# Kernel optimization log

Hardware: AMD Instinct MI355X
Metric: run time of the kernel (lower is better)

## Reference

```python
import jax, jax.numpy as jnp
import numpy as np

N_NODES = 100000
N_EDGES = 1600000
FDIM = 128


def setup_inputs() -> dict:
    key = jax.random.key(0)
    k1, k2 = jax.random.split(key)
    x = jax.random.normal(k1, (N_NODES, FDIM), dtype=jnp.float32)
    edge_index = jax.random.randint(k2, (2, N_EDGES), 0, N_NODES, dtype=jnp.int64)
    # GCNConv params as loaded by the module: identity weight, zero bias
    W = jnp.eye(FDIM, dtype=jnp.float32)
    bias = jnp.zeros((FDIM,), dtype=jnp.float32)
    return {"x": x, "W": W, "bias": bias, "edge_index": edge_index}


def reference(x, W, bias, edge_index):
    n = x.shape[0]
    src, dst = edge_index[0], edge_index[1]
    # GCNConv default: add self-loops with weight 1.0
    loop = jnp.arange(n, dtype=edge_index.dtype)
    src_f = jnp.concatenate([src, loop])
    dst_f = jnp.concatenate([dst, loop])
    ew = jnp.ones(src_f.shape[0], dtype=x.dtype)
    # symmetric normalization: deg computed on destination (col)
    deg = jax.ops.segment_sum(ew, dst_f, num_segments=n)
    dinv = jnp.where(deg > 0, deg ** -0.5, 0.0).astype(x.dtype)
    norm = dinv[src_f] * dinv[dst_f]  # [E+n]
    h = x @ W.T  # linear transform (W = I here, but kept faithful)
    msg = h[src_f] * norm[:, None]  # gather + scale, [E+n, fdim]
    out = jax.ops.segment_sum(msg, dst_f, num_segments=n) + bias  # scatter-add
    return jnp.sum(out, axis=0, keepdims=True)  # [1, fdim]
```

## Files before the change

### kernel.cpp

```cpp
#include <hip/hip_runtime.h>

#define FD 128
#define CHD 32768
#define NSLD 64
#define CHS 16384
#define NSLS 32
#define RXB 512
#define QSCALE 16777216.0f
#define QINV   5.9604644775390625e-8f

__device__ __forceinline__ unsigned quant_w(int dp1) {
    return (unsigned)(rsqrtf((float)dp1) * QSCALE + 0.5f);
}

__device__ __forceinline__ bool detect_is32_wave(const unsigned int* w, long long nwords) {
    const int lane = threadIdx.x & 63;
    const long long i0 = 2 * lane + 1, i1 = 2 * (lane + 64) + 1;
    unsigned acc = 0;
    if (i0 < nwords) acc |= w[i0];
    if (i1 < nwords) acc |= w[i1];
    return __ballot(acc != 0u) != 0ull;
}

__device__ __forceinline__ int4 ld_e4(const void* ei, bool is32, long long off, long long i) {
    if (is32) return *reinterpret_cast<const int4*>((const int*)ei + off + i);
    const long long* p = (const long long*)ei + off + i;
    longlong2 a = *reinterpret_cast<const longlong2*>(p);
    longlong2 b = *reinterpret_cast<const longlong2*>(p + 2);
    return make_int4((int)a.x, (int)a.y, (int)b.x, (int)b.y);
}
__device__ __forceinline__ int ld_e1(const void* ei, bool is32, long long idx) {
    return is32 ? ((const int*)ei)[idx] : (int)((const long long*)ei)[idx];
}

__global__ __launch_bounds__(512) void hist_deg_kernel(
        const void* __restrict__ ei, unsigned int* __restrict__ psD,
        long long E, long long SL, int nch) {
    __shared__ unsigned int hist[CHD / 2];
    const int tid = threadIdx.x;
    const bool is32 = detect_is32_wave((const unsigned int*)ei, 2 * E);
    const int b = blockIdx.x, c = b % nch, j = b / nch;
    const int lo = c * CHD;
    for (int i = tid; i < CHD / 2; i += 512) hist[i] = 0u;
    __syncthreads();
    const long long e0 = (long long)j * SL;
    long long e1 = e0 + SL; if (e1 > E) e1 = E; if (e1 < e0) e1 = e0;
    const long long e1v = e0 + ((e1 - e0) & ~3LL);
    for (long long i = e0 + (long long)tid * 4; i < e1v; i += 2048) {
        int4 d = ld_e4(ei, is32, E, i);
        unsigned u0 = (unsigned)(d.x - lo), u1 = (unsigned)(d.y - lo);
        unsigned u2 = (unsigned)(d.z - lo), u3 = (unsigned)(d.w - lo);
        if (u0 < CHD) atomicAdd(&hist[u0 >> 1], 1u << ((u0 & 1) * 16));
        if (u1 < CHD) atomicAdd(&hist[u1 >> 1], 1u << ((u1 & 1) * 16));
        if (u2 < CHD) atomicAdd(&hist[u2 >> 1], 1u << ((u2 & 1) * 16));
        if (u3 < CHD) atomicAdd(&hist[u3 >> 1], 1u << ((u3 & 1) * 16));
    }
    { long long it = e1v + tid;
      if (it < e1) { unsigned u = (unsigned)(ld_e1(ei, is32, E + it) - lo);
                     if (u < CHD) atomicAdd(&hist[u >> 1], 1u << ((u & 1) * 16)); } }
    __syncthreads();
    unsigned int* o = psD + (size_t)b * (CHD / 2);
    for (int w = tid; w < CHD / 2; w += 512) o[w] = hist[w];
}

__global__ void deg_reduce_kernel(const unsigned int* __restrict__ psD,
                                  int* __restrict__ deg, long long n, int nch) {
    const long long tw = blockIdx.x * (long long)blockDim.x + threadIdx.x;
    if (tw >= (long long)nch * (CHD / 2)) return;
    const int cc = (int)(tw / (CHD / 2));
    const int w  = (int)(tw % (CHD / 2));
    unsigned s0 = 0, s1 = 0;
    for (int j = 0; j < NSLD; ++j) {
        unsigned v = psD[((size_t)j * nch + cc) * (CHD / 2) + w];
        s0 += v & 0xffffu; s1 += v >> 16;
    }
    const long long v0 = (long long)cc * CHD + 2 * w;
    if (v0 < n) deg[v0] = (int)s0;
    if (v0 + 1 < n) deg[v0 + 1] = (int)s1;
}

__global__ __launch_bounds__(512) void hist_s_kernel(
        const void* __restrict__ ei, const int* __restrict__ deg,
        unsigned int* __restrict__ psS, long long E, long long SL, int nch) {
    __shared__ unsigned int hist[CHS];
    const int tid = threadIdx.x;
    const bool is32 = detect_is32_wave((const unsigned int*)ei, 2 * E);
    const int b = blockIdx.x, c = b % nch, j = b / nch;
    const int lo = c * CHS;
    for (int i = tid; i < CHS; i += 512) hist[i] = 0u;
    __syncthreads();
    const long long e0 = (long long)j * SL;
    long long e1 = e0 + SL; if (e1 > E) e1 = E; if (e1 < e0) e1 = e0;
    const long long e1v = e0 + ((e1 - e0) & ~3LL);
    for (long long i = e0 + (long long)tid * 4; i < e1v; i += 2048) {
        int4 s = ld_e4(ei, is32, 0, i);
        int4 d = ld_e4(ei, is32, E, i);
        unsigned u0 = (unsigned)(s.x - lo), u1 = (unsigned)(s.y - lo);
        unsigned u2 = (unsigned)(s.z - lo), u3 = (unsigned)(s.w - lo);
        if (u0 < CHS) atomicAdd(&hist[u0], quant_w(deg[d.x] + 1));
        if (u1 < CHS) atomicAdd(&hist[u1], quant_w(deg[d.y] + 1));
        if (u2 < CHS) atomicAdd(&hist[u2], quant_w(deg[d.z] + 1));
        if (u3 < CHS) atomicAdd(&hist[u3], quant_w(deg[d.w] + 1));
    }
    { long long it = e1v + tid;
      if (it < e1) { unsigned u = (unsigned)(ld_e1(ei, is32, it) - lo);
                     if (u < CHS) atomicAdd(&hist[u], quant_w(deg[ld_e1(ei, is32, E + it)] + 1)); } }
    __syncthreads();
    unsigned int* o = psS + (size_t)b * CHS;
    for (int w = tid; w < CHS; w += 512) o[w] = hist[w];
}

__global__ void coef_reduce_kernel(const unsigned int* __restrict__ psS,
                                   const int* __restrict__ deg,
                                   float* __restrict__ coef, long long n, int nch) {
    const long long v = blockIdx.x * (long long)blockDim.x + threadIdx.x;
    if (v >= n) return;
    const int cc = (int)(v / CHS);
    const int u  = (int)(v % CHS);
    unsigned s = 0;
    #pragma unroll 8
    for (int jj = 0; jj < NSLS; ++jj)
        s += psS[((size_t)jj * nch + cc) * CHS + u];
    const float dg = (float)(deg[v] + 1);
    const float di = rsqrtf(dg);
    coef[v] = di * ((float)s * QINV) + 1.0f / dg;
}

__global__ __launch_bounds__(256) void reduce_x_kernel(
        const float* __restrict__ x, const float* __restrict__ coef,
        float* __restrict__ P, long long n) {
    __shared__ float4 sm4[256];
    const int tid = threadIdx.x;
    float4 a = make_float4(0.f, 0.f, 0.f, 0.f);
    const long long tot = n * (FD / 4);
    for (long long i = blockIdx.x * 256LL + tid; i < tot; i += (long long)RXB * 256) {
        float cf = coef[i >> 5];
        float4 xv = reinterpret_cast<const float4*>(x)[i];
        a.x += cf * xv.x; a.y += cf * xv.y; a.z += cf * xv.z; a.w += cf * xv.w;
    }
    const int lane = tid & 31, grp = tid >> 5;
    sm4[grp * 32 + lane] = a;
    __syncthreads();
    for (int s2 = 4; s2 > 0; s2 >>= 1) {
        if (grp < s2) {
            float4 o = sm4[(grp + s2) * 32 + lane];
            float4 m = sm4[grp * 32 + lane];
            m.x += o.x; m.y += o.y; m.z += o.z; m.w += o.w;
            sm4[grp * 32 + lane] = m;
        }
        __syncthreads();
    }
    if (tid < 32) reinterpret_cast<float4*>(P)[blockIdx.x * 32 + tid] = sm4[tid];
}

__global__ __launch_bounds__(256) void colsum_final_kernel(
        const float* __restrict__ P, const float* __restrict__ Wm,
        const float* __restrict__ bias, float* __restrict__ out, float nn) {
    __shared__ float wrow[FD];
    __shared__ float red[256];
    const int f = blockIdx.x, tid = threadIdx.x;
    if (tid < FD) wrow[tid] = Wm[f * FD + tid];
    __syncthreads();
    float part = 0.f;
    for (int j = tid; j < RXB; j += 256) {
        const float4* Pj = reinterpret_cast<const float4*>(P + (size_t)j * FD);
        #pragma unroll
        for (int k = 0; k < FD / 4; ++k) {
            float4 p = Pj[k];
            part += wrow[4 * k] * p.x + wrow[4 * k + 1] * p.y +
                    wrow[4 * k + 2] * p.z + wrow[4 * k + 3] * p.w;
        }
    }
    red[tid] = part;
    __syncthreads();
    for (int s2 = 128; s2 > 0; s2 >>= 1) {
        if (tid < s2) red[tid] += red[tid + s2];
        __syncthreads();
    }
    if (tid == 0) out[f] = red[0] + nn * bias[f];
}

__global__ void deg_fb(const void* __restrict__ ei, int* __restrict__ deg, long long E) {
    const bool is32 = detect_is32_wave((const unsigned int*)ei, 2 * E);
    const long long st = (long long)gridDim.x * blockDim.x;
    long long i = blockIdx.x * (long long)blockDim.x + threadIdx.x;
    for (; i < E; i += st) atomicAdd(&deg[ld_e1(ei, is32, E + i)], 1);
}

__global__ void srcsum_fb(const void* __restrict__ ei, const int* __restrict__ deg,
                          unsigned int* __restrict__ Sq, long long E) {
    const bool is32 = detect_is32_wave((const unsigned int*)ei, 2 * E);
    const long long st = (long long)gridDim.x * blockDim.x;
    long long i = blockIdx.x * (long long)blockDim.x + threadIdx.x;
    for (; i < E; i += st)
        atomicAdd(&Sq[ld_e1(ei, is32, i)], quant_w(deg[ld_e1(ei, is32, E + i)] + 1));
}

__global__ void coef_fb(unsigned int* __restrict__ Sq, const int* __restrict__ deg,
                        long long n) {
    const long long v = blockIdx.x * (long long)blockDim.x + threadIdx.x;
    if (v >= n) return;
    unsigned s = Sq[v];
    float dg = (float)(deg[v] + 1);
    float di = rsqrtf(dg);
    ((float*)Sq)[v] = di * ((float)s * QINV) + 1.0f / dg;
}

__global__ void redx_fb(const float* __restrict__ x, const float* __restrict__ coef,
                        float* __restrict__ t, long long n) {
    __shared__ float sm[FD];
    for (int f = threadIdx.x; f < FD; f += blockDim.x) sm[f] = 0.f;
    __syncthreads();
    const long long tot = n * (FD / 4);
    const long long st = (long long)gridDim.x * blockDim.x;
    const int lane = threadIdx.x & 31;
    float4 a = make_float4(0.f, 0.f, 0.f, 0.f);
    for (long long i = blockIdx.x * (long long)blockDim.x + threadIdx.x; i < tot; i += st) {
        float cf = coef[i >> 5];
        float4 xv = reinterpret_cast<const float4*>(x)[i];
        a.x += cf * xv.x; a.y += cf * xv.y; a.z += cf * xv.z; a.w += cf * xv.w;
    }
    atomicAdd(&sm[lane * 4 + 0], a.x);
    atomicAdd(&sm[lane * 4 + 1], a.y);
    atomicAdd(&sm[lane * 4 + 2], a.z);
    atomicAdd(&sm[lane * 4 + 3], a.w);
    __syncthreads();
    for (int f = threadIdx.x; f < FD; f += blockDim.x) atomicAdd(&t[f], sm[f]);
}

__global__ void final_fb(const float* __restrict__ Wm, const float* __restrict__ bias,
                         const float* __restrict__ t, float* __restrict__ out, float nn) {
    __shared__ float ts[FD];
    int f = threadIdx.x;
    if (f < FD) ts[f] = t[f];
    __syncthreads();
    if (f < FD) {
        float a0 = 0.f;
        #pragma unroll 16
        for (int k = 0; k < FD; ++k) a0 += Wm[f * FD + k] * ts[k];
        out[f] = a0 + nn * bias[f];
    }
}

extern "C" void kernel_launch(void* const* d_in, const int* in_sizes, int n_in,
                              void* d_out, int out_size, void* d_ws, size_t ws_size,
                              hipStream_t stream) {
    const float* x    = (const float*)d_in[0];
    const float* W    = (const float*)d_in[1];
    const float* bias = (const float*)d_in[2];
    const void*  ei   = d_in[3];
    float* out = (float*)d_out;
    const long long n = in_sizes[0] / FD;
    const long long E = (long long)in_sizes[3] / 2;

    const int NCHD = (int)((n + CHD - 1) / CHD);
    const int NCHS = (int)((n + CHS - 1) / CHS);
    const long long SLD = ((E + NSLD - 1) / NSLD + 3) & ~3LL;
    const long long SLS = ((E + NSLS - 1) / NSLS + 3) & ~3LL;

    char* ws = (char*)d_ws;
    size_t off = 0;
    auto take = [&](size_t bytes) { size_t r = off; off += (bytes + 255) & ~(size_t)255; return r; };
    unsigned int* psD  = (unsigned int*)(ws + take((size_t)NCHD * NSLD * (CHD / 2) * 4));
    unsigned int* psS  = (unsigned int*)(ws + take((size_t)NCHS * NSLS * CHS * 4));
    int*          deg  = (int*)(ws + take((size_t)n * 4));
    float*        coef = (float*)(ws + take((size_t)n * 4));
    float*        P    = (float*)(ws + take((size_t)RXB * FD * 4));
    const size_t need = off;

    const bool main_ok = (ws_size >= need) && ((E & 3) == 0) && (E >= 512) &&
                         (SLD < 65536);

    if (main_ok) {
        hist_deg_kernel<<<NCHD * NSLD, 512, 0, stream>>>(ei, psD, E, SLD, NCHD);
        {
            long long nw = (long long)NCHD * (CHD / 2);
            deg_reduce_kernel<<<(int)((nw + 255) / 256), 256, 0, stream>>>(psD, deg, n, NCHD);
        }
        hist_s_kernel<<<NCHS * NSLS, 512, 0, stream>>>(ei, deg, psS, E, SLS, NCHS);
        coef_reduce_kernel<<<(int)((n + 255) / 256), 256, 0, stream>>>(psS, deg, coef, n, NCHS);
        reduce_x_kernel<<<RXB, 256, 0, stream>>>(x, coef, P, n);
        colsum_final_kernel<<<FD, 256, 0, stream>>>(P, W, bias, out, (float)n);
    } else {
        int*          degF = (int*)ws;
        unsigned int* Sq   = (unsigned int*)(ws + (size_t)n * 4);
        float*        tF   = (float*)(ws + (size_t)n * 8);
        hipMemsetAsync(ws, 0, (size_t)n * 8 + 512, stream);
        deg_fb<<<1600, 256, 0, stream>>>(ei, degF, E);
        srcsum_fb<<<1600, 256, 0, stream>>>(ei, degF, Sq, E);
        coef_fb<<<(int)((n + 255) / 256), 256, 0, stream>>>(Sq, degF, n);
        redx_fb<<<2048, 256, 0, stream>>>(x, (const float*)Sq, tF, n);
        final_fb<<<1, FD, 0, stream>>>(W, bias, tF, out, (float)n);
    }
}
```

Baseline: 87.39 us.

## Precompute 16-bit per-edge dst weights once instead of per source chunk

Adds a kernel that computes a quantized 16-bit rsqrt(deg+1) weight per edge once. The source histogram kernel then reads this compact array instead of re-loading dst indices and doing random deg gathers plus rsqrt in every chunk pass (NCHS passes over all edges). The quantization scale drops from 2^24 to 2^15, which loses precision in the coefficients, and the number of edge slices doubles. The cost is one extra launch and an E*2-byte workspace buffer.

```diff
diff --git a/kernel.cpp b/kernel.cpp
--- a/kernel.cpp
+++ b/kernel.cpp
@@ -4,13 +4,18 @@
 #define CHD 32768
 #define NSLD 64
 #define CHS 16384
-#define NSLS 32
+#define NSLS 64
 #define RXB 512
 #define QSCALE 16777216.0f
 #define QINV   5.9604644775390625e-8f
+#define QSCALE2 32768.0f
+#define QINV2  3.0517578125e-5f
 
 __device__ __forceinline__ unsigned quant_w(int dp1) {
     return (unsigned)(rsqrtf((float)dp1) * QSCALE + 0.5f);
+}
+__device__ __forceinline__ unsigned short quant_w16(int dp1) {
+    return (unsigned short)(rsqrtf((float)dp1) * QSCALE2 + 0.5f);
 }
 
 __device__ __forceinline__ bool detect_is32_wave(const unsigned int* w, long long nwords) {
@@ -79,8 +84,30 @@
     if (v0 + 1 < n) deg[v0 + 1] = (int)s1;
 }
 
+__global__ __launch_bounds__(256) void qw_kernel(
+        const void* __restrict__ ei, const int* __restrict__ deg,
+        unsigned short* __restrict__ qw, long long E) {
+    const bool is32 = detect_is32_wave((const unsigned int*)ei, 2 * E);
+    const long long stride4 = (long long)gridDim.x * blockDim.x * 4;
+    const long long E4 = E & ~3LL;
+    for (long long i = (blockIdx.x * (long long)blockDim.x + threadIdx.x) * 4;
+         i < E4; i += stride4) {
+        int4 d = ld_e4(ei, is32, E, i);
+        ushort4 q;
+        q.x = quant_w16(deg[d.x] + 1);
+        q.y = quant_w16(deg[d.y] + 1);
+        q.z = quant_w16(deg[d.z] + 1);
+        q.w = quant_w16(deg[d.w] + 1);
+        *reinterpret_cast<ushort4*>(qw + i) = q;
+    }
+    const long long st1 = (long long)gridDim.x * blockDim.x;
+    for (long long k = E4 + blockIdx.x * (long long)blockDim.x + threadIdx.x;
+         k < E; k += st1)
+        qw[k] = quant_w16(deg[ld_e1(ei, is32, E + k)] + 1);
+}
+
 __global__ __launch_bounds__(512) void hist_s_kernel(
-        const void* __restrict__ ei, const int* __restrict__ deg,
+        const void* __restrict__ ei, const unsigned short* __restrict__ qw,
         unsigned int* __restrict__ psS, long long E, long long SL, int nch) {
     __shared__ unsigned int hist[CHS];
     const int tid = threadIdx.x;
@@ -94,17 +121,17 @@
     const long long e1v = e0 + ((e1 - e0) & ~3LL);
     for (long long i = e0 + (long long)tid * 4; i < e1v; i += 2048) {
         int4 s = ld_e4(ei, is32, 0, i);
-        int4 d = ld_e4(ei, is32, E, i);
+        ushort4 q = *reinterpret_cast<const ushort4*>(qw + i);
         unsigned u0 = (unsigned)(s.x - lo), u1 = (unsigned)(s.y - lo);
         unsigned u2 = (unsigned)(s.z - lo), u3 = (unsigned)(s.w - lo);
-        if (u0 < CHS) atomicAdd(&hist[u0], quant_w(deg[d.x] + 1));
-        if (u1 < CHS) atomicAdd(&hist[u1], quant_w(deg[d.y] + 1));
-        if (u2 < CHS) atomicAdd(&hist[u2], quant_w(deg[d.z] + 1));
-        if (u3 < CHS) atomicAdd(&hist[u3], quant_w(deg[d.w] + 1));
+        if (u0 < CHS) atomicAdd(&hist[u0], (unsigned)q.x);
+        if (u1 < CHS) atomicAdd(&hist[u1], (unsigned)q.y);
+        if (u2 < CHS) atomicAdd(&hist[u2], (unsigned)q.z);
+        if (u3 < CHS) atomicAdd(&hist[u3], (unsigned)q.w);
     }
     { long long it = e1v + tid;
       if (it < e1) { unsigned u = (unsigned)(ld_e1(ei, is32, it) - lo);
-                     if (u < CHS) atomicAdd(&hist[u], quant_w(deg[ld_e1(ei, is32, E + it)] + 1)); } }
+                     if (u < CHS) atomicAdd(&hist[u], (unsigned)qw[it]); } }
     __syncthreads();
     unsigned int* o = psS + (size_t)b * CHS;
     for (int w = tid; w < CHS; w += 512) o[w] = hist[w];
@@ -123,7 +150,7 @@
         s += psS[((size_t)jj * nch + cc) * CHS + u];
     const float dg = (float)(deg[v] + 1);
     const float di = rsqrtf(dg);
-    coef[v] = di * ((float)s * QINV) + 1.0f / dg;
+    coef[v] = di * ((float)s * QINV2) + 1.0f / dg;
 }
 
 __global__ __launch_bounds__(256) void reduce_x_kernel(
@@ -261,11 +288,12 @@
     char* ws = (char*)d_ws;
     size_t off = 0;
     auto take = [&](size_t bytes) { size_t r = off; off += (bytes + 255) & ~(size_t)255; return r; };
-    unsigned int* psD  = (unsigned int*)(ws + take((size_t)NCHD * NSLD * (CHD / 2) * 4));
-    unsigned int* psS  = (unsigned int*)(ws + take((size_t)NCHS * NSLS * CHS * 4));
-    int*          deg  = (int*)(ws + take((size_t)n * 4));
-    float*        coef = (float*)(ws + take((size_t)n * 4));
-    float*        P    = (float*)(ws + take((size_t)RXB * FD * 4));
+    unsigned int*   psD  = (unsigned int*)(ws + take((size_t)NCHD * NSLD * (CHD / 2) * 4));
+    unsigned int*   psS  = (unsigned int*)(ws + take((size_t)NCHS * NSLS * CHS * 4));
+    int*            deg  = (int*)(ws + take((size_t)n * 4));
+    float*          coef = (float*)(ws + take((size_t)n * 4));
+    unsigned short* qw   = (unsigned short*)(ws + take((size_t)E * 2));
+    float*          P    = (float*)(ws + take((size_t)RXB * FD * 4));
     const size_t need = off;
 
     const bool main_ok = (ws_size >= need) && ((E & 3) == 0) && (E >= 512) &&
@@ -277,7 +305,8 @@
             long long nw = (long long)NCHD * (CHD / 2);
             deg_reduce_kernel<<<(int)((nw + 255) / 256), 256, 0, stream>>>(psD, deg, n, NCHD);
         }
-        hist_s_kernel<<<NCHS * NSLS, 512, 0, stream>>>(ei, deg, psS, E, SLS, NCHS);
+        qw_kernel<<<1024, 256, 0, stream>>>(ei, deg, qw, E);
+        hist_s_kernel<<<NCHS * NSLS, 512, 0, stream>>>(ei, qw, psS, E, SLS, NCHS);
         coef_reduce_kernel<<<(int)((n + 255) / 256), 256, 0, stream>>>(psS, deg, coef, n, NCHS);
         reduce_x_kernel<<<RXB, 256, 0, stream>>>(x, coef, P, n);
         colsum_final_kernel<<<FD, 256, 0, stream>>>(P, W, bias, out, (float)n);
```

New measurement: 77.78 us. 1.12x faster.

## Prepack quantized weight with source index and fuse coef into x reduction

Applied to the files above, without the earlier changes.

Adds a pass that computes each edge's quantized dinv[dst] once and packs it with the 17-bit source index into a single 32-bit word. The chunked source histogram kernel then reads one packed stream instead of re-reading src/dst indices and gathering deg in every chunk pass. The coefficient reduction is also folded into the x-reduction kernel, with each block computing coefs for its contiguous node range in shared memory, which removes one launch and the coef buffer. In exchange it adds an E-sized workspace, drops weight precision to 14 bits, and restricts the main path to n up to 2^17.

```diff
diff --git a/kernel.cpp b/kernel.cpp
--- a/kernel.cpp
+++ b/kernel.cpp
@@ -8,9 +8,15 @@
 #define RXB 512
 #define QSCALE 16777216.0f
 #define QINV   5.9604644775390625e-8f
+#define QS14   16384.0f
+#define QI14   6.103515625e-5f
+#define SRCMASK 0x1FFFFu
 
 __device__ __forceinline__ unsigned quant_w(int dp1) {
     return (unsigned)(rsqrtf((float)dp1) * QSCALE + 0.5f);
+}
+__device__ __forceinline__ unsigned quant_w14(int dp1) {
+    return (unsigned)(rsqrtf((float)dp1) * QS14 + 0.5f);
 }
 
 __device__ __forceinline__ bool detect_is32_wave(const unsigned int* w, long long nwords) {
@@ -79,12 +85,35 @@
     if (v0 + 1 < n) deg[v0 + 1] = (int)s1;
 }
 
+__global__ __launch_bounds__(256) void qwpack_kernel(
+        const void* __restrict__ ei, const int* __restrict__ deg,
+        unsigned int* __restrict__ qp, long long E) {
+    const bool is32 = detect_is32_wave((const unsigned int*)ei, 2 * E);
+    const long long stride4 = (long long)gridDim.x * blockDim.x * 4;
+    const long long E4 = E & ~3LL;
+    for (long long i = (blockIdx.x * (long long)blockDim.x + threadIdx.x) * 4;
+         i < E4; i += stride4) {
+        int4 s = ld_e4(ei, is32, 0, i);
+        int4 d = ld_e4(ei, is32, E, i);
+        uint4 q;
+        q.x = (quant_w14(deg[d.x] + 1) << 17) | (unsigned)s.x;
+        q.y = (quant_w14(deg[d.y] + 1) << 17) | (unsigned)s.y;
+        q.z = (quant_w14(deg[d.z] + 1) << 17) | (unsigned)s.z;
+        q.w = (quant_w14(deg[d.w] + 1) << 17) | (unsigned)s.w;
+        *reinterpret_cast<uint4*>(qp + i) = q;
+    }
+    const long long st1 = (long long)gridDim.x * blockDim.x;
+    for (long long k = E4 + blockIdx.x * (long long)blockDim.x + threadIdx.x;
+         k < E; k += st1)
+        qp[k] = (quant_w14(deg[ld_e1(ei, is32, E + k)] + 1) << 17) |
+                (unsigned)ld_e1(ei, is32, k);
+}
+
 __global__ __launch_bounds__(512) void hist_s_kernel(
-        const void* __restrict__ ei, const int* __restrict__ deg,
-        unsigned int* __restrict__ psS, long long E, long long SL, int nch) {
+        const unsigned int* __restrict__ qp, unsigned int* __restrict__ psS,
+        long long E, long long SL, int nch) {
     __shared__ unsigned int hist[CHS];
     const int tid = threadIdx.x;
-    const bool is32 = detect_is32_wave((const unsigned int*)ei, 2 * E);
     const int b = blockIdx.x, c = b % nch, j = b / nch;
     const int lo = c * CHS;
     for (int i = tid; i < CHS; i += 512) hist[i] = 0u;
@@ -93,49 +122,51 @@
     long long e1 = e0 + SL; if (e1 > E) e1 = E; if (e1 < e0) e1 = e0;
     const long long e1v = e0 + ((e1 - e0) & ~3LL);
     for (long long i = e0 + (long long)tid * 4; i < e1v; i += 2048) {
-        int4 s = ld_e4(ei, is32, 0, i);
-        int4 d = ld_e4(ei, is32, E, i);
-        unsigned u0 = (unsigned)(s.x - lo), u1 = (unsigned)(s.y - lo);
-        unsigned u2 = (unsigned)(s.z - lo), u3 = (unsigned)(s.w - lo);
-        if (u0 < CHS) atomicAdd(&hist[u0], quant_w(deg[d.x] + 1));
-        if (u1 < CHS) atomicAdd(&hist[u1], quant_w(deg[d.y] + 1));
-        if (u2 < CHS) atomicAdd(&hist[u2], quant_w(deg[d.z] + 1));
-        if (u3 < CHS) atomicAdd(&hist[u3], quant_w(deg[d.w] + 1));
+        uint4 p = *reinterpret_cast<const uint4*>(qp + i);
+        unsigned u0 = (p.x & SRCMASK) - lo, u1 = (p.y & SRCMASK) - lo;
+        unsigned u2 = (p.z & SRCMASK) - lo, u3 = (p.w & SRCMASK) - lo;
+        if (u0 < CHS) atomicAdd(&hist[u0], p.x >> 17);
+        if (u1 < CHS) atomicAdd(&hist[u1], p.y >> 17);
+        if (u2 < CHS) atomicAdd(&hist[u2], p.z >> 17);
+        if (u3 < CHS) atomicAdd(&hist[u3], p.w >> 17);
     }
     { long long it = e1v + tid;
-      if (it < e1) { unsigned u = (unsigned)(ld_e1(ei, is32, it) - lo);
-                     if (u < CHS) atomicAdd(&hist[u], quant_w(deg[ld_e1(ei, is32, E + it)] + 1)); } }
+      if (it < e1) { unsigned p = qp[it];
+                     unsigned u = (p & SRCMASK) - lo;
+                     if (u < CHS) atomicAdd(&hist[u], p >> 17); } }
     __syncthreads();
     unsigned int* o = psS + (size_t)b * CHS;
     for (int w = tid; w < CHS; w += 512) o[w] = hist[w];
 }
 
-__global__ void coef_reduce_kernel(const unsigned int* __restrict__ psS,
-                                   const int* __restrict__ deg,
-                                   float* __restrict__ coef, long long n, int nch) {
-    const long long v = blockIdx.x * (long long)blockDim.x + threadIdx.x;
-    if (v >= n) return;
-    const int cc = (int)(v / CHS);
-    const int u  = (int)(v % CHS);
-    unsigned s = 0;
-    #pragma unroll 8
-    for (int jj = 0; jj < NSLS; ++jj)
-        s += psS[((size_t)jj * nch + cc) * CHS + u];
-    const float dg = (float)(deg[v] + 1);
-    const float di = rsqrtf(dg);
-    coef[v] = di * ((float)s * QINV) + 1.0f / dg;
-}
-
-__global__ __launch_bounds__(256) void reduce_x_kernel(
-        const float* __restrict__ x, const float* __restrict__ coef,
-        float* __restrict__ P, long long n) {
+__global__ __launch_bounds__(256) void reduce_x_coef_kernel(
+        const float* __restrict__ x, const int* __restrict__ deg,
+        const unsigned int* __restrict__ psS, float* __restrict__ P,
+        long long n, int nch) {
+    __shared__ float lcoef[1024];
     __shared__ float4 sm4[256];
     const int tid = threadIdx.x;
+    const long long vlo = (long long)blockIdx.x * n / RXB;
+    const long long vhi = ((long long)blockIdx.x + 1) * n / RXB;
+    const int nv = (int)(vhi - vlo);
+    for (int t = tid; t < nv; t += 256) {
+        const long long v = vlo + t;
+        const int cc = (int)(v / CHS);
+        const int u  = (int)(v % CHS);
+        unsigned s = 0;
+        #pragma unroll 8
+        for (int jj = 0; jj < NSLS; ++jj)
+            s += psS[((size_t)jj * nch + cc) * CHS + u];
+        const float dg = (float)(deg[v] + 1);
+        const float di = rsqrtf(dg);
+        lcoef[t] = di * ((float)s * QI14) + 1.0f / dg;
+    }
+    __syncthreads();
     float4 a = make_float4(0.f, 0.f, 0.f, 0.f);
-    const long long tot = n * (FD / 4);
-    for (long long i = blockIdx.x * 256LL + tid; i < tot; i += (long long)RXB * 256) {
-        float cf = coef[i >> 5];
-        float4 xv = reinterpret_cast<const float4*>(x)[i];
+    const long long i0 = vlo * (FD / 4), i1 = vhi * (FD / 4);
+    for (long long i = i0 + tid; i < i1; i += 256) {
+        const float cf = lcoef[(int)((i >> 5) - vlo)];
+        const float4 xv = reinterpret_cast<const float4*>(x)[i];
         a.x += cf * xv.x; a.y += cf * xv.y; a.z += cf * xv.z; a.w += cf * xv.w;
     }
     const int lane = tid & 31, grp = tid >> 5;
@@ -261,15 +292,16 @@
     char* ws = (char*)d_ws;
     size_t off = 0;
     auto take = [&](size_t bytes) { size_t r = off; off += (bytes + 255) & ~(size_t)255; return r; };
-    unsigned int* psD  = (unsigned int*)(ws + take((size_t)NCHD * NSLD * (CHD / 2) * 4));
-    unsigned int* psS  = (unsigned int*)(ws + take((size_t)NCHS * NSLS * CHS * 4));
-    int*          deg  = (int*)(ws + take((size_t)n * 4));
-    float*        coef = (float*)(ws + take((size_t)n * 4));
-    float*        P    = (float*)(ws + take((size_t)RXB * FD * 4));
+    unsigned int* psD = (unsigned int*)(ws + take((size_t)NCHD * NSLD * (CHD / 2) * 4));
+    unsigned int* psS = (unsigned int*)(ws + take((size_t)NCHS * NSLS * CHS * 4));
+    int*          deg = (int*)(ws + take((size_t)n * 4));
+    unsigned int* qp  = (unsigned int*)(ws + take((size_t)E * 4));
+    float*        P   = (float*)(ws + take((size_t)RXB * FD * 4));
     const size_t need = off;
 
     const bool main_ok = (ws_size >= need) && ((E & 3) == 0) && (E >= 512) &&
-                         (SLD < 65536);
+                         (SLD < 65536) && (n <= (1LL << 17)) &&
+                         (n <= (long long)RXB * 1024);
 
     if (main_ok) {
         hist_deg_kernel<<<NCHD * NSLD, 512, 0, stream>>>(ei, psD, E, SLD, NCHD);
@@ -277,9 +309,9 @@
             long long nw = (long long)NCHD * (CHD / 2);
             deg_reduce_kernel<<<(int)((nw + 255) / 256), 256, 0, stream>>>(psD, deg, n, NCHD);
         }
-        hist_s_kernel<<<NCHS * NSLS, 512, 0, stream>>>(ei, deg, psS, E, SLS, NCHS);
-        coef_reduce_kernel<<<(int)((n + 255) / 256), 256, 0, stream>>>(psS, deg, coef, n, NCHS);
-        reduce_x_kernel<<<RXB, 256, 0, stream>>>(x, coef, P, n);
+        qwpack_kernel<<<1024, 256, 0, stream>>>(ei, deg, qp, E);
+        hist_s_kernel<<<NCHS * NSLS, 512, 0, stream>>>(qp, psS, E, SLS, NCHS);
+        reduce_x_coef_kernel<<<RXB, 256, 0, stream>>>(x, deg, psS, P, n, NCHS);
         colsum_final_kernel<<<FD, 256, 0, stream>>>(P, W, bias, out, (float)n);
     } else {
         int*          degF = (int*)ws;
```

Result: faster. 73.27 us (-16.2%).
